# Performance work log

Hardware: AMD Instinct MI355X
Metric: run time of the kernel (lower is better)

## Reference

```python
import jax, jax.numpy as jnp
import numpy as np

N = 100000      # nodes
E = 1600000     # edges (avg degree 16)
D_IN, D_H, D_OUT = 128, 128, 64


def _pow(d, e):
    # torch code zeroes out inf from 0 ** negative_exponent
    p = jnp.power(d, e)
    return jnp.where(jnp.isinf(p), jnp.zeros_like(p), p)


def _gso_weights(params, deg, row, col):
    # params = [m1, m2, m3, e1, e2, e3, a]
    m1, m2, m3, e1, e2, e3, a = (params[i] for i in range(7))
    d = deg + a                       # self-loop-adjusted degrees, [N]
    pe2 = _pow(d, e2)
    pe3 = _pow(d, e3)
    w_edge = m2 * pe2[row] * pe3[col]                     # off-diagonal GSO entries, [E]
    w_self = m1 * _pow(d, e1) + m2 * pe2 * pe3 + m3       # diagonal GSO entries, [N]
    return w_edge, w_self


def setup_inputs() -> dict:
    key = jax.random.key(0)
    ks = jax.random.split(key, 8)
    x = jax.random.normal(ks[0], (N, D_IN), dtype=jnp.float32)
    edge_index = jax.random.randint(ks[1], (2, E), 0, N, dtype=jnp.int32)
    glorot = lambda k, i, o: jax.random.normal(k, (i, o), dtype=jnp.float32) * np.float32(np.sqrt(2.0 / (i + o)))
    W1 = glorot(ks[2], D_IN, D_H)
    W2 = glorot(ks[3], D_H, D_H)
    W3 = glorot(ks[4], D_H, D_OUT)
    b1 = jnp.zeros((D_H,), jnp.float32)
    b2 = jnp.zeros((D_H,), jnp.float32)
    b3 = jnp.zeros((D_OUT,), jnp.float32)
    # [m1, m2, m3, e1, e2, e3, a]
    gso1_params = jnp.array([0.0, 1.0, 0.0, 0.0, -0.5, -0.5, 1.0], jnp.float32)   # NORMADJ
    gso2_params = jnp.array([0.0, -1.0, 1.0, 0.0, -1.0, 0.0, 0.0], jnp.float32)   # RWLAPLACIAN
    return {"x": x, "edge_index": edge_index, "W1": W1, "b1": b1, "W2": W2,
            "b2": b2, "W3": W3, "b3": b3, "gso1_params": gso1_params,
            "gso2_params": gso2_params}


def reference(x, edge_index, W1, b1, W2, b2, W3, b3, gso1_params, gso2_params):
    row, col = edge_index[0], edge_index[1]
    deg = jax.ops.segment_sum(jnp.ones(row.shape, x.dtype), row, num_segments=N)
    we1, ws1 = _gso_weights(gso1_params, deg, row, col)
    we2, ws2 = _gso_weights(gso2_params, deg, row, col)
    w_edge = we1 + we2   # combined two-GSO edge weights, [E]
    w_self = ws1 + ws2   # combined diagonal (self-loop) weights, [N]

    def conv(h, W, b):
        h = h @ W                                                        # [N, d_out]
        agg = jax.ops.segment_sum(w_edge[:, None] * h[col], row, num_segments=N)
        return agg + w_self[:, None] * h + b

    h = jax.nn.relu(conv(x, W1, b1))
    h = jax.nn.relu(conv(h, W2, b2))   # dropout=0.0 (eval) -> identity
    return conv(h, W3, b3)
```

## Files before the change

kernel.cpp:

```cpp
#include <hip/hip_runtime.h>
#include <hip/hip_fp16.h>
#include <math.h>
#include <type_traits>

typedef _Float16 half8 __attribute__((ext_vector_type(8)));
typedef float floatx4 __attribute__((ext_vector_type(4)));

__global__ void deg_convert_kernel(const int* __restrict__ row, int* __restrict__ degi, int E,
                                   const float* __restrict__ W1, const float* __restrict__ W2,
                                   const float* __restrict__ W3, _Float16* __restrict__ Wt1,
                                   _Float16* __restrict__ Wt2, _Float16* __restrict__ Wt3,
                                   int degBlocks) {
    if ((int)blockIdx.x < degBlocks) {
        int g = blockIdx.x * 256 + threadIdx.x;
        if (g < E) atomicAdd(&degi[row[g]], 1);
    } else {
        int g = (blockIdx.x - degBlocks) * 256 + threadIdx.x;
        if (g < 16384) {
            int k = g >> 7, n = g & 127;
            Wt1[n * 128 + k] = (_Float16)W1[g];
        } else if (g < 32768) {
            int h = g - 16384; int k = h >> 7, n = h & 127;
            Wt2[n * 128 + k] = (_Float16)W2[h];
        } else if (g < 40960) {
            int h = g - 32768; int k = h >> 6, n = h & 63;
            Wt3[n * 128 + k] = (_Float16)W3[h];
        }
    }
}

__device__ __forceinline__ float pow_z(float d, float e) {
    float p = powf(d, e);
    return isinf(p) ? 0.0f : p;
}

__device__ __forceinline__ void gso_coeff(float deg, const float* __restrict__ p1,
                                          const float* __restrict__ p2,
                                          float4* cf, float* ws) {
    float m1a = p1[0], m2a = p1[1], m3a = p1[2], e1a = p1[3], e2a = p1[4], e3a = p1[5], aa = p1[6];
    float m1b = p2[0], m2b = p2[1], m3b = p2[2], e1b = p2[3], e2b = p2[4], e3b = p2[5], ab = p2[6];
    float d1 = deg + aa, d2 = deg + ab;
    float pa1 = pow_z(d1, e1a), pa2 = pow_z(d1, e2a), pa3 = pow_z(d1, e3a);
    float pb1 = pow_z(d2, e1b), pb2 = pow_z(d2, e2b), pb3 = pow_z(d2, e3b);
    *cf = make_float4(m2a * pa2, pa3, m2b * pb2, pb3);
    *ws = m1a * pa1 + m2a * pa2 * pa3 + m3a
        + m1b * pb1 + m2b * pb2 * pb3 + m3b;
}

__global__ void scan_block_kernel(const int* __restrict__ degi, int* __restrict__ rowptr,
                                  int* __restrict__ blocksum,
                                  const float* __restrict__ p1, const float* __restrict__ p2,
                                  float4* __restrict__ coeff, float* __restrict__ wself, int n) {
    __shared__ int sums[256];
    int tid = threadIdx.x;
    int base = blockIdx.x * 1024 + tid * 4;
    int d0 = (base + 0 < n) ? degi[base + 0] : 0;
    int d1 = (base + 1 < n) ? degi[base + 1] : 0;
    int d2 = (base + 2 < n) ? degi[base + 2] : 0;
    int d3 = (base + 3 < n) ? degi[base + 3] : 0;
    int s0 = d0, s1 = s0 + d1, s2 = s1 + d2, s3 = s2 + d3;
    sums[tid] = s3;
    __syncthreads();
    for (int off = 1; off < 256; off <<= 1) {
        int v = (tid >= off) ? sums[tid - off] : 0;
        __syncthreads();
        sums[tid] += v;
        __syncthreads();
    }
    int excl = sums[tid] - s3;
    if (base + 0 < n) rowptr[base + 1] = excl + s0;
    if (base + 1 < n) rowptr[base + 2] = excl + s1;
    if (base + 2 < n) rowptr[base + 3] = excl + s2;
    if (base + 3 < n) rowptr[base + 4] = excl + s3;
    if (tid == 255) blocksum[blockIdx.x] = sums[255];
    int dd[4] = {d0, d1, d2, d3};
#pragma unroll
    for (int u = 0; u < 4; ++u) {
        if (base + u < n) {
            float4 cf; float ws;
            gso_coeff((float)dd[u], p1, p2, &cf, &ws);
            coeff[base + u] = cf;
            wself[base + u] = ws;
        }
    }
}

__global__ void scan_add_kernel(int* __restrict__ rowptr, const int* __restrict__ blocksum,
                                int n, int nblk) {
    __shared__ int s[128];
    int tid = threadIdx.x;
    if (tid < 128) s[tid] = (tid < nblk) ? blocksum[tid] : 0;
    __syncthreads();
    for (int off = 1; off < 128; off <<= 1) {
        int v = 0;
        if (tid < 128 && tid >= off) v = s[tid - off];
        __syncthreads();
        if (tid < 128) s[tid] += v;
        __syncthreads();
    }
    int g = blockIdx.x * 256 + tid;
    if (g == 0) rowptr[0] = 0;
    if (g < n) {
        int b = g >> 10;
        int off = (b == 0) ? 0 : s[b - 1];
        rowptr[g + 1] += off;
    }
}

__global__ __launch_bounds__(256) void partition_kernel(
        const int* __restrict__ row, const int* __restrict__ col,
        const int* __restrict__ rowptr, int* __restrict__ gcur,
        const float4* __restrict__ coeff, int2* __restrict__ epack_mid,
        int E, int shift, int NB) {
    __shared__ int scnt[256], sofs[256], scur[256], gslot[256];
    __shared__ int2 sdata[4096];
    __shared__ unsigned short sbkt[4096];

    int tid = threadIdx.x;
    int base = blockIdx.x * 4096;
    scnt[tid] = 0;
    __syncthreads();

    int epk[16]; float ew[16]; int eb[16];
#pragma unroll
    for (int u = 0; u < 16; ++u) {
        int e = base + u * 256 + tid;
        eb[u] = -1;
        if (e < E) {
            int r = row[e], c = col[e];
            int b = r >> shift;
            eb[u] = b;
            atomicAdd(&scnt[b], 1);
            float4 cr = coeff[r], cc = coeff[c];
            ew[u] = cr.x * cc.y + cr.z * cc.w;
            epk[u] = c | ((r & ((1 << shift) - 1)) << 20);
        }
    }
    __syncthreads();
    sofs[tid] = scnt[tid];
    __syncthreads();
    for (int off = 1; off < 256; off <<= 1) {
        int v = (tid >= off) ? sofs[tid - off] : 0;
        __syncthreads();
        sofs[tid] += v;
        __syncthreads();
    }
    int excl = sofs[tid] - scnt[tid];
    sofs[tid] = excl;
    scur[tid] = excl;
    if (tid < NB && scnt[tid] > 0)
        gslot[tid] = rowptr[tid << shift] + atomicAdd(&gcur[tid], scnt[tid]);
    __syncthreads();
#pragma unroll
    for (int u = 0; u < 16; ++u) {
        if (eb[u] >= 0) {
            int idx = atomicAdd(&scur[eb[u]], 1);
            sdata[idx] = make_int2(epk[u], __float_as_int(ew[u]));
            sbkt[idx] = (unsigned short)eb[u];
        }
    }
    __syncthreads();
    int cntR = min(4096, E - base);
    for (int i = tid; i < cntR; i += 256) {
        int b = sbkt[i];
        epack_mid[gslot[b] + (i - sofs[b])] = sdata[i];
    }
}

__global__ __launch_bounds__(256) void bucket_sort_kernel(
        const int* __restrict__ rowptr, const int2* __restrict__ epack_mid,
        int2* __restrict__ epack, int N, int shift) {
    __shared__ int lcur[4096];
    int b = blockIdx.x;
    int tid = threadIdx.x;
    int rows = 1 << shift;
    int row0 = b << shift;
    for (int j = tid; j < rows; j += 256) {
        int rid = row0 + j;
        if (rid < N) lcur[j] = rowptr[rid];
    }
    __syncthreads();
    int slice0 = rowptr[row0];
    int slice1 = rowptr[min(row0 + rows, N)];
    for (int i = slice0 + tid; i < slice1; i += 256) {
        int2 p = epack_mid[i];
        int rl = ((unsigned)p.x) >> 20;
        int pos = atomicAdd(&lcur[rl], 1);
        epack[pos] = make_int2(p.x & 0xFFFFF, p.y);
    }
}

template<int TN, typename AT>
__global__ __launch_bounds__(256) void gemm_mfma(const AT* __restrict__ A,
        const _Float16* __restrict__ Wt, _Float16* __restrict__ C, int n) {
    constexpr int K = 128;
    constexpr int TM = 128;
    constexpr int LDK = K + 8;
    __shared__ _Float16 As[TM][LDK];
    __shared__ _Float16 Bs[TN][LDK];

    int tid = threadIdx.x;
    int wave = tid >> 6, lane = tid & 63;
    int q = lane >> 4, t = lane & 15;
    int rowbase = blockIdx.x * TM;

    if constexpr (std::is_same<AT, float>::value) {
        for (int i = tid; i < TM * K / 4; i += 256) {
            int r = i >> 5;
            int kc = (i & 31) * 4;
            int rr = rowbase + r;
            float4 v = make_float4(0.f, 0.f, 0.f, 0.f);
            if (rr < n) v = *(const float4*)&A[(size_t)rr * K + kc];
            As[r][kc + 0] = (_Float16)v.x;
            As[r][kc + 1] = (_Float16)v.y;
            As[r][kc + 2] = (_Float16)v.z;
            As[r][kc + 3] = (_Float16)v.w;
        }
    } else {
        for (int i = tid; i < TM * K / 8; i += 256) {
            int r = i >> 4;
            int kc = (i & 15) * 8;
            int rr = rowbase + r;
            uint4 v = make_uint4(0u, 0u, 0u, 0u);
            if (rr < n) v = *(const uint4*)&A[(size_t)rr * K + kc];
            *(uint4*)&As[r][kc] = v;
        }
    }
    for (int i = tid; i < TN * K / 8; i += 256) {
        int nr = i >> 4;
        int kc = (i & 15) * 8;
        *(uint4*)&Bs[nr][kc] = *(const uint4*)&Wt[(size_t)nr * K + kc];
    }
    __syncthreads();

    int m0 = wave * 32;
    floatx4 acc0[TN / 16], acc1[TN / 16];
#pragma unroll
    for (int nt = 0; nt < TN / 16; ++nt) {
        acc0[nt] = (floatx4){0.f, 0.f, 0.f, 0.f};
        acc1[nt] = (floatx4){0.f, 0.f, 0.f, 0.f};
    }

#pragma unroll
    for (int kk = 0; kk < K; kk += 32) {
        half8 a0 = *(const half8*)&As[m0 + t][kk + q * 8];
        half8 a1 = *(const half8*)&As[m0 + 16 + t][kk + q * 8];
#pragma unroll
        for (int nt = 0; nt < TN / 16; ++nt) {
            half8 b = *(const half8*)&Bs[nt * 16 + t][kk + q * 8];
            acc0[nt] = __builtin_amdgcn_mfma_f32_16x16x32_f16(a0, b, acc0[nt], 0, 0, 0);
            acc1[nt] = __builtin_amdgcn_mfma_f32_16x16x32_f16(a1, b, acc1[nt], 0, 0, 0);
        }
    }

#pragma unroll
    for (int nt = 0; nt < TN / 16; ++nt) {
#pragma unroll
        for (int r = 0; r < 4; ++r) {
            int rr0 = rowbase + m0 + q * 4 + r;
            if (rr0 < n) C[(size_t)rr0 * TN + nt * 16 + t] = (_Float16)acc0[nt][r];
            int rr1 = rr0 + 16;
            if (rr1 < n) C[(size_t)rr1 * TN + nt * 16 + t] = (_Float16)acc1[nt][r];
        }
    }
}

__global__ __launch_bounds__(256) void agg128_kernel(const __half2* __restrict__ H,
        const int* __restrict__ rowptr, const int2* __restrict__ epack,
        const float* __restrict__ wself, const float* __restrict__ bias,
        __half2* __restrict__ out, int n) {
    int node = blockIdx.x * 4 + (threadIdx.x >> 6);
    if (node >= n) return;
    int lane = threadIdx.x & 63;
    int start = rowptr[node], end = rowptr[node + 1];
    float ws = wself[node];
    float2 hs = __half22float2(H[(size_t)node * 64 + lane]);
    float ax = ws * hs.x, ay = ws * hs.y;
    int e = start;
    for (; e + 16 <= end; e += 16) {
        int2 p[16];
#pragma unroll
        for (int j = 0; j < 16; ++j) p[j] = epack[e + j];
        __half2 hh[16];
#pragma unroll
        for (int j = 0; j < 16; ++j) hh[j] = H[(size_t)p[j].x * 64 + lane];
#pragma unroll
        for (int j = 0; j < 16; ++j) {
            float w = __int_as_float(p[j].y);
            float2 f = __half22float2(hh[j]);
            ax += w * f.x; ay += w * f.y;
        }
    }
    if (e + 8 <= end) {
        int2 p[8];
#pragma unroll
        for (int j = 0; j < 8; ++j) p[j] = epack[e + j];
        __half2 hh[8];
#pragma unroll
        for (int j = 0; j < 8; ++j) hh[j] = H[(size_t)p[j].x * 64 + lane];
#pragma unroll
        for (int j = 0; j < 8; ++j) {
            float w = __int_as_float(p[j].y);
            float2 f = __half22float2(hh[j]);
            ax += w * f.x; ay += w * f.y;
        }
        e += 8;
    }
    if (e + 4 <= end) {
        int2 p[4];
#pragma unroll
        for (int j = 0; j < 4; ++j) p[j] = epack[e + j];
        __half2 hh[4];
#pragma unroll
        for (int j = 0; j < 4; ++j) hh[j] = H[(size_t)p[j].x * 64 + lane];
#pragma unroll
        for (int j = 0; j < 4; ++j) {
            float w = __int_as_float(p[j].y);
            float2 f = __half22float2(hh[j]);
            ax += w * f.x; ay += w * f.y;
        }
        e += 4;
    }
    for (; e < end; ++e) {
        int2 pe = epack[e];
        float w = __int_as_float(pe.y);
        float2 f = __half22float2(H[(size_t)pe.x * 64 + lane]);
        ax += w * f.x; ay += w * f.y;
    }
    float2 b = *(const float2*)&bias[2 * lane];
    float vx = fmaxf(ax + b.x, 0.0f);
    float vy = fmaxf(ay + b.y, 0.0f);
    out[(size_t)node * 64 + lane] = __floats2half2_rn(vx, vy);
}

__global__ __launch_bounds__(256) void agg64_kernel(const __half* __restrict__ H,
        const int* __restrict__ rowptr, const int2* __restrict__ epack,
        const float* __restrict__ wself, const float* __restrict__ bias,
        float* __restrict__ out, int n) {
    int node = blockIdx.x * 4 + (threadIdx.x >> 6);
    if (node >= n) return;
    int lane = threadIdx.x & 63;
    int start = rowptr[node], end = rowptr[node + 1];
    float ws = wself[node];
    float acc = ws * __half2float(H[(size_t)node * 64 + lane]);
    int e = start;
    for (; e + 16 <= end; e += 16) {
        int2 p[16];
#pragma unroll
        for (int j = 0; j < 16; ++j) p[j] = epack[e + j];
        float f[16];
#pragma unroll
        for (int j = 0; j < 16; ++j) f[j] = __half2float(H[(size_t)p[j].x * 64 + lane]);
#pragma unroll
        for (int j = 0; j < 16; ++j) acc += __int_as_float(p[j].y) * f[j];
    }
    if (e + 8 <= end) {
        int2 p[8];
#pragma unroll
        for (int j = 0; j < 8; ++j) p[j] = epack[e + j];
        float f[8];
#pragma unroll
        for (int j = 0; j < 8; ++j) f[j] = __half2float(H[(size_t)p[j].x * 64 + lane]);
#pragma unroll
        for (int j = 0; j < 8; ++j) acc += __int_as_float(p[j].y) * f[j];
        e += 8;
    }
    if (e + 4 <= end) {
        int2 p[4];
#pragma unroll
        for (int j = 0; j < 4; ++j) p[j] = epack[e + j];
        float f[4];
#pragma unroll
        for (int j = 0; j < 4; ++j) f[j] = __half2float(H[(size_t)p[j].x * 64 + lane]);
#pragma unroll
        for (int j = 0; j < 4; ++j) acc += __int_as_float(p[j].y) * f[j];
        e += 4;
    }
    for (; e < end; ++e) {
        int2 pe = epack[e];
        acc += __int_as_float(pe.y) * __half2float(H[(size_t)pe.x * 64 + lane]);
    }
    out[(size_t)node * 64 + lane] = acc + bias[lane];
}

extern "C" void kernel_launch(void* const* d_in, const int* in_sizes, int n_in,
                              void* d_out, int out_size, void* d_ws, size_t ws_size,
                              hipStream_t stream) {
    const float* x  = (const float*)d_in[0];
    const int*   ei = (const int*)d_in[1];
    const float* W1 = (const float*)d_in[2];
    const float* b1 = (const float*)d_in[3];
    const float* W2 = (const float*)d_in[4];
    const float* b2 = (const float*)d_in[5];
    const float* W3 = (const float*)d_in[6];
    const float* b3 = (const float*)d_in[7];
    const float* p1 = (const float*)d_in[8];
    const float* p2 = (const float*)d_in[9];

    const int N = in_sizes[0] / 128;
    const int E = in_sizes[1] / 2;
    const int* row = ei;
    const int* col = ei + E;

    int shift = 0;
    while ((((N - 1) >> shift) + 1) > 256) shift++;
    const int NB = ((N - 1) >> shift) + 1;

    char* p = (char*)d_ws;
    auto alloc = [&](size_t bytes) -> void* {
        void* q = (void*)p;
        p += (bytes + 255) & ~(size_t)255;
        return q;
    };
    int*      degi      = (int*)alloc((size_t)N * 4);
    int*      gcur      = (int*)alloc(256 * 4);
    int*      rowptr    = (int*)alloc((size_t)(N + 1) * 4);
    const int NBLK      = (N + 1023) / 1024;
    int*      blocksum  = (int*)alloc((size_t)NBLK * 4);
    float4*   coeff     = (float4*)alloc((size_t)N * 16);
    float*    wself     = (float*)alloc((size_t)N * 4);
    int2*     epack_mid = (int2*)alloc((size_t)E * 8);
    int2*     epack     = (int2*)alloc((size_t)E * 8);
    _Float16* Wt1       = (_Float16*)alloc(128 * 128 * 2);
    _Float16* Wt2       = (_Float16*)alloc(128 * 128 * 2);
    _Float16* Wt3       = (_Float16*)alloc(128 * 64 * 2);
    _Float16* bufH      = (_Float16*)alloc((size_t)N * 128 * 2);
    _Float16* actH      = (_Float16*)alloc((size_t)N * 128 * 2);
    (void)ws_size; (void)n_in;

    size_t zero_bytes = (size_t)((char*)rowptr - (char*)degi);
    hipMemsetAsync(degi, 0, zero_bytes, stream);

    const int degBlocks = (E + 255) / 256;
    deg_convert_kernel<<<degBlocks + 160, 256, 0, stream>>>(row, degi, E, W1, W2, W3,
                                                            Wt1, Wt2, Wt3, degBlocks);
    scan_block_kernel<<<NBLK, 256, 0, stream>>>(degi, rowptr, blocksum, p1, p2, coeff, wself, N);
    scan_add_kernel<<<(N + 255) / 256, 256, 0, stream>>>(rowptr, blocksum, N, NBLK);
    partition_kernel<<<(E + 4095) / 4096, 256, 0, stream>>>(row, col, rowptr, gcur, coeff,
                                                            epack_mid, E, shift, NB);
    bucket_sort_kernel<<<NB, 256, 0, stream>>>(rowptr, epack_mid, epack, N, shift);

    float* out = (float*)d_out;
    int aggGrid = (N + 3) / 4;
    int gemmGrid = (N + 127) / 128;
    gemm_mfma<128, float><<<gemmGrid, 256, 0, stream>>>(x, Wt1, bufH, N);
    agg128_kernel<<<aggGrid, 256, 0, stream>>>((const __half2*)bufH, rowptr, epack, wself,
                                               b1, (__half2*)actH, N);
    gemm_mfma<128, _Float16><<<gemmGrid, 256, 0, stream>>>(actH, Wt2, bufH, N);
    agg128_kernel<<<aggGrid, 256, 0, stream>>>((const __half2*)bufH, rowptr, epack, wself,
                                               b2, (__half2*)actH, N);
    gemm_mfma<64, _Float16><<<gemmGrid, 256, 0, stream>>>(actH, Wt3, bufH, N);
    agg64_kernel<<<aggGrid, 256, 0, stream>>>((const __half*)bufH, rowptr, epack, wself,
                                              b3, out, N);
}
```

Baseline: 487.2 us.

## Fuse first GEMM into setup kernel with degree count and weight conversion

After: 485.8 us. About the same (-0.3%).

```diff
diff --git a/kernel.cpp b/kernel.cpp
--- a/kernel.cpp
+++ b/kernel.cpp
@@ -6,27 +6,136 @@
 typedef _Float16 half8 __attribute__((ext_vector_type(8)));
 typedef float floatx4 __attribute__((ext_vector_type(4)));
 
-__global__ void deg_convert_kernel(const int* __restrict__ row, int* __restrict__ degi, int E,
-                                   const float* __restrict__ W1, const float* __restrict__ W2,
-                                   const float* __restrict__ W3, _Float16* __restrict__ Wt1,
-                                   _Float16* __restrict__ Wt2, _Float16* __restrict__ Wt3,
-                                   int degBlocks) {
-    if ((int)blockIdx.x < degBlocks) {
-        int g = blockIdx.x * 256 + threadIdx.x;
-        if (g < E) atomicAdd(&degi[row[g]], 1);
+template<int TN, typename AT, bool WFP32>
+__device__ __forceinline__ void gemm_body(const AT* __restrict__ A,
+        const void* __restrict__ Wsrc, _Float16* __restrict__ C, int n, int blk,
+        _Float16* lds) {
+    constexpr int K = 128;
+    constexpr int TM = 128;
+    constexpr int LDK = K + 8;
+    _Float16 (*As)[LDK] = (_Float16 (*)[LDK])lds;
+    _Float16 (*Bs)[LDK] = (_Float16 (*)[LDK])(lds + TM * LDK);
+
+    int tid = threadIdx.x;
+    int wave = tid >> 6, lane = tid & 63;
+    int q = lane >> 4, t = lane & 15;
+    int rowbase = blk * TM;
+
+    if constexpr (std::is_same<AT, float>::value) {
+        for (int i = tid; i < TM * K / 4; i += 256) {
+            int r = i >> 5;
+            int kc = (i & 31) * 4;
+            int rr = rowbase + r;
+            float4 v = make_float4(0.f, 0.f, 0.f, 0.f);
+            if (rr < n) v = *(const float4*)&A[(size_t)rr * K + kc];
+            As[r][kc + 0] = (_Float16)v.x;
+            As[r][kc + 1] = (_Float16)v.y;
+            As[r][kc + 2] = (_Float16)v.z;
+            As[r][kc + 3] = (_Float16)v.w;
+        }
     } else {
-        int g = (blockIdx.x - degBlocks) * 256 + threadIdx.x;
+        for (int i = tid; i < TM * K / 8; i += 256) {
+            int r = i >> 4;
+            int kc = (i & 15) * 8;
+            int rr = rowbase + r;
+            uint4 v = make_uint4(0u, 0u, 0u, 0u);
+            if (rr < n) v = *(const uint4*)&A[(size_t)rr * K + kc];
+            *(uint4*)&As[r][kc] = v;
+        }
+    }
+    if constexpr (WFP32) {
+        const float* W = (const float*)Wsrc;
+        for (int i = tid; i < K * TN / 4; i += 256) {
+            float4 v = *(const float4*)&W[i * 4];
+            int k = (i * 4) / TN, nn = (i * 4) % TN;
+            Bs[nn + 0][k] = (_Float16)v.x;
+            Bs[nn + 1][k] = (_Float16)v.y;
+            Bs[nn + 2][k] = (_Float16)v.z;
+            Bs[nn + 3][k] = (_Float16)v.w;
+        }
+    } else {
+        const _Float16* Wt = (const _Float16*)Wsrc;
+        for (int i = tid; i < TN * K / 8; i += 256) {
+            int nr = i >> 4;
+            int kc = (i & 15) * 8;
+            *(uint4*)&Bs[nr][kc] = *(const uint4*)&Wt[(size_t)nr * K + kc];
+        }
+    }
+    __syncthreads();
+
+    int m0 = wave * 32;
+    floatx4 acc0[TN / 16], acc1[TN / 16];
+#pragma unroll
+    for (int nt = 0; nt < TN / 16; ++nt) {
+        acc0[nt] = (floatx4){0.f, 0.f, 0.f, 0.f};
+        acc1[nt] = (floatx4){0.f, 0.f, 0.f, 0.f};
+    }
+
+#pragma unroll
+    for (int kk = 0; kk < K; kk += 32) {
+        half8 a0 = *(const half8*)&As[m0 + t][kk + q * 8];
+        half8 a1 = *(const half8*)&As[m0 + 16 + t][kk + q * 8];
+#pragma unroll
+        for (int nt = 0; nt < TN / 16; ++nt) {
+            half8 b = *(const half8*)&Bs[nt * 16 + t][kk + q * 8];
+            acc0[nt] = __builtin_amdgcn_mfma_f32_16x16x32_f16(a0, b, acc0[nt], 0, 0, 0);
+            acc1[nt] = __builtin_amdgcn_mfma_f32_16x16x32_f16(a1, b, acc1[nt], 0, 0, 0);
+        }
+    }
+
+#pragma unroll
+    for (int nt = 0; nt < TN / 16; ++nt) {
+#pragma unroll
+        for (int r = 0; r < 4; ++r) {
+            int rr0 = rowbase + m0 + q * 4 + r;
+            if (rr0 < n) C[(size_t)rr0 * TN + nt * 16 + t] = (_Float16)acc0[nt][r];
+            int rr1 = rr0 + 16;
+            if (rr1 < n) C[(size_t)rr1 * TN + nt * 16 + t] = (_Float16)acc1[nt][r];
+        }
+    }
+}
+
+__global__ __launch_bounds__(256) void setup_fused_kernel(
+        const float* __restrict__ x, const float* __restrict__ W1,
+        _Float16* __restrict__ bufH, int N,
+        const int* __restrict__ row, int* __restrict__ degi, int E,
+        const float* __restrict__ W2, const float* __restrict__ W3,
+        _Float16* __restrict__ Wt2, _Float16* __restrict__ Wt3,
+        int gemmBlocks, int degBlocks4) {
+    __shared__ _Float16 lds[(128 + 128) * 136];
+    int b = blockIdx.x;
+    if (b < gemmBlocks) {
+        gemm_body<128, float, true>(x, W1, bufH, N, b, lds);
+    } else if (b < gemmBlocks + degBlocks4) {
+        int e0 = (b - gemmBlocks) * 1024 + threadIdx.x * 4;
+        if (e0 + 3 < E) {
+            int4 r4 = *(const int4*)&row[e0];
+            atomicAdd(&degi[r4.x], 1);
+            atomicAdd(&degi[r4.y], 1);
+            atomicAdd(&degi[r4.z], 1);
+            atomicAdd(&degi[r4.w], 1);
+        } else {
+#pragma unroll
+            for (int j = 0; j < 4; ++j)
+                if (e0 + j < E) atomicAdd(&degi[row[e0 + j]], 1);
+        }
+    } else {
+        int g = (b - gemmBlocks - degBlocks4) * 256 + threadIdx.x;
         if (g < 16384) {
             int k = g >> 7, n = g & 127;
-            Wt1[n * 128 + k] = (_Float16)W1[g];
-        } else if (g < 32768) {
-            int h = g - 16384; int k = h >> 7, n = h & 127;
-            Wt2[n * 128 + k] = (_Float16)W2[h];
-        } else if (g < 40960) {
-            int h = g - 32768; int k = h >> 6, n = h & 63;
+            Wt2[n * 128 + k] = (_Float16)W2[g];
+        } else if (g < 24576) {
+            int h = g - 16384; int k = h >> 6, n = h & 63;
             Wt3[n * 128 + k] = (_Float16)W3[h];
         }
     }
+}
+
+template<int TN>
+__global__ __launch_bounds__(256) void gemm_mfma(const _Float16* __restrict__ A,
+        const _Float16* __restrict__ Wt, _Float16* __restrict__ C, int n) {
+    __shared__ _Float16 lds[(128 + TN) * 136];
+    gemm_body<TN, _Float16, false>(A, Wt, C, n, blockIdx.x, lds);
 }
 
 __device__ __forceinline__ float pow_z(float d, float e) {
@@ -112,7 +221,7 @@
         const int* __restrict__ rowptr, int* __restrict__ gcur,
         const float4* __restrict__ coeff, int2* __restrict__ epack_mid,
         int E, int shift, int NB) {
-    __shared__ int scnt[256], sofs[256], scur[256], gslot[256];
+    __shared__ int scnt[256], sofs[256], gslot[256];
     __shared__ int2 sdata[4096];
     __shared__ unsigned short sbkt[4096];
 
@@ -121,16 +230,30 @@
     scnt[tid] = 0;
     __syncthreads();
 
-    int epk[16]; float ew[16]; int eb[16];
-#pragma unroll
-    for (int u = 0; u < 16; ++u) {
-        int e = base + u * 256 + tid;
-        eb[u] = -1;
-        if (e < E) {
-            int r = row[e], c = col[e];
+    int epk[16]; float ew[16]; int eb[16]; int eidx[16];
+#pragma unroll
+    for (int v = 0; v < 4; ++v) {
+        int e0 = base + v * 1024 + tid * 4;
+        int4 r4, c4;
+        bool full = (e0 + 3 < E);
+        if (full) {
+            r4 = *(const int4*)&row[e0];
+            c4 = *(const int4*)&col[e0];
+        }
+#pragma unroll
+        for (int j = 0; j < 4; ++j) {
+            int u = v * 4 + j;
+            eb[u] = -1;
+            int r, c;
+            if (full) {
+                r = (&r4.x)[j]; c = (&c4.x)[j];
+            } else {
+                if (e0 + j >= E) continue;
+                r = row[e0 + j]; c = col[e0 + j];
+            }
             int b = r >> shift;
             eb[u] = b;
-            atomicAdd(&scnt[b], 1);
+            eidx[u] = atomicAdd(&scnt[b], 1);
             float4 cr = coeff[r], cc = coeff[c];
             ew[u] = cr.x * cc.y + cr.z * cc.w;
             epk[u] = c | ((r & ((1 << shift) - 1)) << 20);
@@ -147,14 +270,13 @@
     }
     int excl = sofs[tid] - scnt[tid];
     sofs[tid] = excl;
-    scur[tid] = excl;
     if (tid < NB && scnt[tid] > 0)
         gslot[tid] = rowptr[tid << shift] + atomicAdd(&gcur[tid], scnt[tid]);
     __syncthreads();
 #pragma unroll
     for (int u = 0; u < 16; ++u) {
         if (eb[u] >= 0) {
-            int idx = atomicAdd(&scur[eb[u]], 1);
+            int idx = sofs[eb[u]] + eidx[u];
             sdata[idx] = make_int2(epk[u], __float_as_int(ew[u]));
             sbkt[idx] = (unsigned short)eb[u];
         }
@@ -187,81 +309,6 @@
         int rl = ((unsigned)p.x) >> 20;
         int pos = atomicAdd(&lcur[rl], 1);
         epack[pos] = make_int2(p.x & 0xFFFFF, p.y);
-    }
-}
-
-template<int TN, typename AT>
-__global__ __launch_bounds__(256) void gemm_mfma(const AT* __restrict__ A,
-        const _Float16* __restrict__ Wt, _Float16* __restrict__ C, int n) {
-    constexpr int K = 128;
-    constexpr int TM = 128;
-    constexpr int LDK = K + 8;
-    __shared__ _Float16 As[TM][LDK];
-    __shared__ _Float16 Bs[TN][LDK];
-
-    int tid = threadIdx.x;
-    int wave = tid >> 6, lane = tid & 63;
-    int q = lane >> 4, t = lane & 15;
-    int rowbase = blockIdx.x * TM;
-
-    if constexpr (std::is_same<AT, float>::value) {
-        for (int i = tid; i < TM * K / 4; i += 256) {
-            int r = i >> 5;
-            int kc = (i & 31) * 4;
-            int rr = rowbase + r;
-            float4 v = make_float4(0.f, 0.f, 0.f, 0.f);
-            if (rr < n) v = *(const float4*)&A[(size_t)rr * K + kc];
-            As[r][kc + 0] = (_Float16)v.x;
-            As[r][kc + 1] = (_Float16)v.y;
-            As[r][kc + 2] = (_Float16)v.z;
-            As[r][kc + 3] = (_Float16)v.w;
-        }
-    } else {
-        for (int i = tid; i < TM * K / 8; i += 256) {
-            int r = i >> 4;
-            int kc = (i & 15) * 8;
-            int rr = rowbase + r;
-            uint4 v = make_uint4(0u, 0u, 0u, 0u);
-            if (rr < n) v = *(const uint4*)&A[(size_t)rr * K + kc];
-            *(uint4*)&As[r][kc] = v;
-        }
-    }
-    for (int i = tid; i < TN * K / 8; i += 256) {
-        int nr = i >> 4;
-        int kc = (i & 15) * 8;
-        *(uint4*)&Bs[nr][kc] = *(const uint4*)&Wt[(size_t)nr * K + kc];
-    }
-    __syncthreads();
-
-    int m0 = wave * 32;
-    floatx4 acc0[TN / 16], acc1[TN / 16];
-#pragma unroll
-    for (int nt = 0; nt < TN / 16; ++nt) {
-        acc0[nt] = (floatx4){0.f, 0.f, 0.f, 0.f};
-        acc1[nt] = (floatx4){0.f, 0.f, 0.f, 0.f};
-    }
-
-#pragma unroll
-    for (int kk = 0; kk < K; kk += 32) {
-        half8 a0 = *(const half8*)&As[m0 + t][kk + q * 8];
-        half8 a1 = *(const half8*)&As[m0 + 16 + t][kk + q * 8];
-#pragma unroll
-        for (int nt = 0; nt < TN / 16; ++nt) {
-            half8 b = *(const half8*)&Bs[nt * 16 + t][kk + q * 8];
-            acc0[nt] = __builtin_amdgcn_mfma_f32_16x16x32_f16(a0, b, acc0[nt], 0, 0, 0);
-            acc1[nt] = __builtin_amdgcn_mfma_f32_16x16x32_f16(a1, b, acc1[nt], 0, 0, 0);
-        }
-    }
-
-#pragma unroll
-    for (int nt = 0; nt < TN / 16; ++nt) {
-#pragma unroll
-        for (int r = 0; r < 4; ++r) {
-            int rr0 = rowbase + m0 + q * 4 + r;
-            if (rr0 < n) C[(size_t)rr0 * TN + nt * 16 + t] = (_Float16)acc0[nt][r];
-            int rr1 = rr0 + 16;
-            if (rr1 < n) C[(size_t)rr1 * TN + nt * 16 + t] = (_Float16)acc1[nt][r];
-        }
     }
 }
 
@@ -421,7 +468,6 @@
     float*    wself     = (float*)alloc((size_t)N * 4);
     int2*     epack_mid = (int2*)alloc((size_t)E * 8);
     int2*     epack     = (int2*)alloc((size_t)E * 8);
-    _Float16* Wt1       = (_Float16*)alloc(128 * 128 * 2);
     _Float16* Wt2       = (_Float16*)alloc(128 * 128 * 2);
     _Float16* Wt3       = (_Float16*)alloc(128 * 64 * 2);
     _Float16* bufH      = (_Float16*)alloc((size_t)N * 128 * 2);
@@ -431,9 +477,12 @@
     size_t zero_bytes = (size_t)((char*)rowptr - (char*)degi);
     hipMemsetAsync(degi, 0, zero_bytes, stream);
 
-    const int degBlocks = (E + 255) / 256;
-    deg_convert_kernel<<<degBlocks + 160, 256, 0, stream>>>(row, degi, E, W1, W2, W3,
-                                                            Wt1, Wt2, Wt3, degBlocks);
+    const int gemmGrid  = (N + 127) / 128;
+    const int degBlocks4 = (E + 1023) / 1024;
+    const int convBlocks = (24576 + 255) / 256;
+    setup_fused_kernel<<<gemmGrid + degBlocks4 + convBlocks, 256, 0, stream>>>(
+        x, W1, bufH, N, row, degi, E, W2, W3, Wt2, Wt3, gemmGrid, degBlocks4);
+
     scan_block_kernel<<<NBLK, 256, 0, stream>>>(degi, rowptr, blocksum, p1, p2, coeff, wself, N);
     scan_add_kernel<<<(N + 255) / 256, 256, 0, stream>>>(rowptr, blocksum, N, NBLK);
     partition_kernel<<<(E + 4095) / 4096, 256, 0, stream>>>(row, col, rowptr, gcur, coeff,
@@ -442,14 +491,12 @@
 
     float* out = (float*)d_out;
     int aggGrid = (N + 3) / 4;
-    int gemmGrid = (N + 127) / 128;
-    gemm_mfma<128, float><<<gemmGrid, 256, 0, stream>>>(x, Wt1, bufH, N);
     agg128_kernel<<<aggGrid, 256, 0, stream>>>((const __half2*)bufH, rowptr, epack, wself,
                                                b1, (__half2*)actH, N);
-    gemm_mfma<128, _Float16><<<gemmGrid, 256, 0, stream>>>(actH, Wt2, bufH, N);
+    gemm_mfma<128><<<gemmGrid, 256, 0, stream>>>(actH, Wt2, bufH, N);
     agg128_kernel<<<aggGrid, 256, 0, stream>>>((const __half2*)bufH, rowptr, epack, wself,
                                                b2, (__half2*)actH, N);
-    gemm_mfma<64, _Float16><<<gemmGrid, 256, 0, stream>>>(actH, Wt3, bufH, N);
+    gemm_mfma<64><<<gemmGrid, 256, 0, stream>>>(actH, Wt3, bufH, N);
     agg64_kernel<<<aggGrid, 256, 0, stream>>>((const __half*)bufH, rowptr, epack, wself,
                                               b3, out, N);
 }
```

## Restructure CSR build around coarse row-bucket histogram instead of per-node degree atomics

Applied to the files above, without the earlier changes.

Result: faster. 428.5 us (-12.0%).

```diff
diff --git a/kernel.cpp b/kernel.cpp
--- a/kernel.cpp
+++ b/kernel.cpp
@@ -6,27 +6,168 @@
 typedef _Float16 half8 __attribute__((ext_vector_type(8)));
 typedef float floatx4 __attribute__((ext_vector_type(4)));
 
-__global__ void deg_convert_kernel(const int* __restrict__ row, int* __restrict__ degi, int E,
-                                   const float* __restrict__ W1, const float* __restrict__ W2,
-                                   const float* __restrict__ W3, _Float16* __restrict__ Wt1,
-                                   _Float16* __restrict__ Wt2, _Float16* __restrict__ Wt3,
-                                   int degBlocks) {
-    if ((int)blockIdx.x < degBlocks) {
-        int g = blockIdx.x * 256 + threadIdx.x;
-        if (g < E) atomicAdd(&degi[row[g]], 1);
+#define RSHIFT 9
+
+__global__ __launch_bounds__(256) void hist_conv_kernel(
+        const int* __restrict__ row, int E, int* __restrict__ bucketsize,
+        const float* __restrict__ W1, const float* __restrict__ W2,
+        const float* __restrict__ W3, _Float16* __restrict__ Wt1,
+        _Float16* __restrict__ Wt2, _Float16* __restrict__ Wt3, int histBlocks) {
+    int tid = threadIdx.x;
+    if ((int)blockIdx.x < histBlocks) {
+        __shared__ int h[256];
+        h[tid] = 0;
+        __syncthreads();
+        int base = blockIdx.x * 16384;
+#pragma unroll
+        for (int it = 0; it < 16; ++it) {
+            int e0 = base + it * 1024 + tid * 4;
+            if (e0 + 3 < E) {
+                int4 r4 = *(const int4*)&row[e0];
+                atomicAdd(&h[r4.x >> RSHIFT], 1);
+                atomicAdd(&h[r4.y >> RSHIFT], 1);
+                atomicAdd(&h[r4.z >> RSHIFT], 1);
+                atomicAdd(&h[r4.w >> RSHIFT], 1);
+            } else {
+#pragma unroll
+                for (int j = 0; j < 4; ++j)
+                    if (e0 + j < E) atomicAdd(&h[row[e0 + j] >> RSHIFT], 1);
+            }
+        }
+        __syncthreads();
+        if (h[tid]) atomicAdd(&bucketsize[tid], h[tid]);
     } else {
-        int g = (blockIdx.x - degBlocks) * 256 + threadIdx.x;
+        int g = ((int)blockIdx.x - histBlocks) * 256 + tid;
         if (g < 16384) {
             int k = g >> 7, n = g & 127;
             Wt1[n * 128 + k] = (_Float16)W1[g];
         } else if (g < 32768) {
-            int h = g - 16384; int k = h >> 7, n = h & 127;
-            Wt2[n * 128 + k] = (_Float16)W2[h];
+            int h2 = g - 16384; int k = h2 >> 7, n = h2 & 127;
+            Wt2[n * 128 + k] = (_Float16)W2[h2];
         } else if (g < 40960) {
-            int h = g - 32768; int k = h >> 6, n = h & 63;
-            Wt3[n * 128 + k] = (_Float16)W3[h];
-        }
-    }
+            int h2 = g - 32768; int k = h2 >> 6, n = h2 & 63;
+            Wt3[n * 128 + k] = (_Float16)W3[h2];
+        }
+    }
+}
+
+__global__ void scan_buckets_kernel(const int* __restrict__ bucketsize,
+                                    int* __restrict__ bucketbase,
+                                    int* __restrict__ rowptr, int N, int E) {
+    __shared__ int s[256];
+    int tid = threadIdx.x;
+    int v = bucketsize[tid];
+    s[tid] = v;
+    __syncthreads();
+    for (int off = 1; off < 256; off <<= 1) {
+        int u = (tid >= off) ? s[tid - off] : 0;
+        __syncthreads();
+        s[tid] += u;
+        __syncthreads();
+    }
+    bucketbase[tid] = s[tid] - v;
+    if (tid == 255) bucketbase[256] = s[255];
+    if (tid == 0) rowptr[N] = E;
+}
+
+__global__ __launch_bounds__(256) void partition_kernel(
+        const int* __restrict__ row, const int* __restrict__ col,
+        const int* __restrict__ bucketbase, int* __restrict__ gcur,
+        int* __restrict__ emid, int E, int NB) {
+    __shared__ int scnt[256], sofs[256], gslot[256];
+    __shared__ int sdata[4096];
+    __shared__ unsigned short sbkt[4096];
+
+    int tid = threadIdx.x;
+    int base = blockIdx.x * 4096;
+    scnt[tid] = 0;
+    __syncthreads();
+
+    int epk[16]; int eb[16]; int eidx[16];
+#pragma unroll
+    for (int v = 0; v < 4; ++v) {
+        int e0 = base + v * 1024 + tid * 4;
+        int4 r4, c4;
+        bool full = (e0 + 3 < E);
+        if (full) {
+            r4 = *(const int4*)&row[e0];
+            c4 = *(const int4*)&col[e0];
+        }
+#pragma unroll
+        for (int j = 0; j < 4; ++j) {
+            int u = v * 4 + j;
+            eb[u] = -1;
+            int r, c;
+            if (full) {
+                r = (&r4.x)[j]; c = (&c4.x)[j];
+            } else {
+                if (e0 + j >= E) continue;
+                r = row[e0 + j]; c = col[e0 + j];
+            }
+            int b = r >> RSHIFT;
+            eb[u] = b;
+            eidx[u] = atomicAdd(&scnt[b], 1);
+            epk[u] = c | ((r & ((1 << RSHIFT) - 1)) << 20);
+        }
+    }
+    __syncthreads();
+    sofs[tid] = scnt[tid];
+    __syncthreads();
+    for (int off = 1; off < 256; off <<= 1) {
+        int v = (tid >= off) ? sofs[tid - off] : 0;
+        __syncthreads();
+        sofs[tid] += v;
+        __syncthreads();
+    }
+    int excl = sofs[tid] - scnt[tid];
+    sofs[tid] = excl;
+    if (tid < NB && scnt[tid] > 0)
+        gslot[tid] = bucketbase[tid] + atomicAdd(&gcur[tid], scnt[tid]);
+    __syncthreads();
+#pragma unroll
+    for (int u = 0; u < 16; ++u) {
+        if (eb[u] >= 0) {
+            int idx = sofs[eb[u]] + eidx[u];
+            sdata[idx] = epk[u];
+            sbkt[idx] = (unsigned short)eb[u];
+        }
+    }
+    __syncthreads();
+    int cntR = min(4096, E - base);
+    for (int i = tid; i < cntR; i += 256) {
+        int b = sbkt[i];
+        emid[gslot[b] + (i - sofs[b])] = sdata[i];
+    }
+}
+
+__global__ __launch_bounds__(256) void bucket_deg_kernel(
+        const int* __restrict__ bucketbase, const int* __restrict__ emid,
+        int* __restrict__ rowptr, int N) {
+    __shared__ int cnt[512];
+    __shared__ int ssum[256];
+    int b = blockIdx.x;
+    int tid = threadIdx.x;
+    int row0 = b << RSHIFT;
+    int nrows = min(512, N - row0);
+    cnt[tid] = 0; cnt[tid + 256] = 0;
+    __syncthreads();
+    int seg0 = bucketbase[b], seg1 = bucketbase[b + 1];
+    for (int i = seg0 + tid; i < seg1; i += 256)
+        atomicAdd(&cnt[((unsigned)emid[i]) >> 20], 1);
+    __syncthreads();
+    int a0 = cnt[2 * tid], a1 = cnt[2 * tid + 1];
+    int tsum = a0 + a1;
+    ssum[tid] = tsum;
+    __syncthreads();
+    for (int off = 1; off < 256; off <<= 1) {
+        int v = (tid >= off) ? ssum[tid - off] : 0;
+        __syncthreads();
+        ssum[tid] += v;
+        __syncthreads();
+    }
+    int excl = ssum[tid] - tsum;
+    if (2 * tid < nrows)     rowptr[row0 + 2 * tid]     = seg0 + excl;
+    if (2 * tid + 1 < nrows) rowptr[row0 + 2 * tid + 1] = seg0 + excl + a0;
 }
 
 __device__ __forceinline__ float pow_z(float d, float e) {
@@ -34,159 +175,51 @@
     return isinf(p) ? 0.0f : p;
 }
 
-__device__ __forceinline__ void gso_coeff(float deg, const float* __restrict__ p1,
-                                          const float* __restrict__ p2,
-                                          float4* cf, float* ws) {
+__global__ void node_coeff_kernel(const int* __restrict__ rowptr,
+                                  const float* __restrict__ p1, const float* __restrict__ p2,
+                                  float4* __restrict__ coeff, float* __restrict__ wself, int N) {
+    int g = blockIdx.x * blockDim.x + threadIdx.x;
+    if (g >= N) return;
+    float deg = (float)(rowptr[g + 1] - rowptr[g]);
     float m1a = p1[0], m2a = p1[1], m3a = p1[2], e1a = p1[3], e2a = p1[4], e3a = p1[5], aa = p1[6];
     float m1b = p2[0], m2b = p2[1], m3b = p2[2], e1b = p2[3], e2b = p2[4], e3b = p2[5], ab = p2[6];
     float d1 = deg + aa, d2 = deg + ab;
     float pa1 = pow_z(d1, e1a), pa2 = pow_z(d1, e2a), pa3 = pow_z(d1, e3a);
     float pb1 = pow_z(d2, e1b), pb2 = pow_z(d2, e2b), pb3 = pow_z(d2, e3b);
-    *cf = make_float4(m2a * pa2, pa3, m2b * pb2, pb3);
-    *ws = m1a * pa1 + m2a * pa2 * pa3 + m3a
-        + m1b * pb1 + m2b * pb2 * pb3 + m3b;
-}
-
-__global__ void scan_block_kernel(const int* __restrict__ degi, int* __restrict__ rowptr,
-                                  int* __restrict__ blocksum,
-                                  const float* __restrict__ p1, const float* __restrict__ p2,
-                                  float4* __restrict__ coeff, float* __restrict__ wself, int n) {
-    __shared__ int sums[256];
-    int tid = threadIdx.x;
-    int base = blockIdx.x * 1024 + tid * 4;
-    int d0 = (base + 0 < n) ? degi[base + 0] : 0;
-    int d1 = (base + 1 < n) ? degi[base + 1] : 0;
-    int d2 = (base + 2 < n) ? degi[base + 2] : 0;
-    int d3 = (base + 3 < n) ? degi[base + 3] : 0;
-    int s0 = d0, s1 = s0 + d1, s2 = s1 + d2, s3 = s2 + d3;
-    sums[tid] = s3;
-    __syncthreads();
-    for (int off = 1; off < 256; off <<= 1) {
-        int v = (tid >= off) ? sums[tid - off] : 0;
-        __syncthreads();
-        sums[tid] += v;
-        __syncthreads();
-    }
-    int excl = sums[tid] - s3;
-    if (base + 0 < n) rowptr[base + 1] = excl + s0;
-    if (base + 1 < n) rowptr[base + 2] = excl + s1;
-    if (base + 2 < n) rowptr[base + 3] = excl + s2;
-    if (base + 3 < n) rowptr[base + 4] = excl + s3;
-    if (tid == 255) blocksum[blockIdx.x] = sums[255];
-    int dd[4] = {d0, d1, d2, d3};
-#pragma unroll
-    for (int u = 0; u < 4; ++u) {
-        if (base + u < n) {
-            float4 cf; float ws;
-            gso_coeff((float)dd[u], p1, p2, &cf, &ws);
-            coeff[base + u] = cf;
-            wself[base + u] = ws;
-        }
-    }
-}
-
-__global__ void scan_add_kernel(int* __restrict__ rowptr, const int* __restrict__ blocksum,
-                                int n, int nblk) {
-    __shared__ int s[128];
-    int tid = threadIdx.x;
-    if (tid < 128) s[tid] = (tid < nblk) ? blocksum[tid] : 0;
-    __syncthreads();
-    for (int off = 1; off < 128; off <<= 1) {
-        int v = 0;
-        if (tid < 128 && tid >= off) v = s[tid - off];
-        __syncthreads();
-        if (tid < 128) s[tid] += v;
-        __syncthreads();
-    }
-    int g = blockIdx.x * 256 + tid;
-    if (g == 0) rowptr[0] = 0;
-    if (g < n) {
-        int b = g >> 10;
-        int off = (b == 0) ? 0 : s[b - 1];
-        rowptr[g + 1] += off;
-    }
-}
-
-__global__ __launch_bounds__(256) void partition_kernel(
-        const int* __restrict__ row, const int* __restrict__ col,
-        const int* __restrict__ rowptr, int* __restrict__ gcur,
-        const float4* __restrict__ coeff, int2* __restrict__ epack_mid,
-        int E, int shift, int NB) {
-    __shared__ int scnt[256], sofs[256], scur[256], gslot[256];
-    __shared__ int2 sdata[4096];
-    __shared__ unsigned short sbkt[4096];
-
-    int tid = threadIdx.x;
-    int base = blockIdx.x * 4096;
-    scnt[tid] = 0;
-    __syncthreads();
-
-    int epk[16]; float ew[16]; int eb[16];
-#pragma unroll
-    for (int u = 0; u < 16; ++u) {
-        int e = base + u * 256 + tid;
-        eb[u] = -1;
-        if (e < E) {
-            int r = row[e], c = col[e];
-            int b = r >> shift;
-            eb[u] = b;
-            atomicAdd(&scnt[b], 1);
-            float4 cr = coeff[r], cc = coeff[c];
-            ew[u] = cr.x * cc.y + cr.z * cc.w;
-            epk[u] = c | ((r & ((1 << shift) - 1)) << 20);
-        }
-    }
-    __syncthreads();
-    sofs[tid] = scnt[tid];
-    __syncthreads();
-    for (int off = 1; off < 256; off <<= 1) {
-        int v = (tid >= off) ? sofs[tid - off] : 0;
-        __syncthreads();
-        sofs[tid] += v;
-        __syncthreads();
-    }
-    int excl = sofs[tid] - scnt[tid];
-    sofs[tid] = excl;
-    scur[tid] = excl;
-    if (tid < NB && scnt[tid] > 0)
-        gslot[tid] = rowptr[tid << shift] + atomicAdd(&gcur[tid], scnt[tid]);
-    __syncthreads();
-#pragma unroll
-    for (int u = 0; u < 16; ++u) {
-        if (eb[u] >= 0) {
-            int idx = atomicAdd(&scur[eb[u]], 1);
-            sdata[idx] = make_int2(epk[u], __float_as_int(ew[u]));
-            sbkt[idx] = (unsigned short)eb[u];
-        }
-    }
-    __syncthreads();
-    int cntR = min(4096, E - base);
-    for (int i = tid; i < cntR; i += 256) {
-        int b = sbkt[i];
-        epack_mid[gslot[b] + (i - sofs[b])] = sdata[i];
-    }
-}
-
-__global__ __launch_bounds__(256) void bucket_sort_kernel(
-        const int* __restrict__ rowptr, const int2* __restrict__ epack_mid,
-        int2* __restrict__ epack, int N, int shift) {
-    __shared__ int lcur[4096];
+    coeff[g] = make_float4(m2a * pa2, pa3, m2b * pb2, pb3);
+    wself[g] = m1a * pa1 + m2a * pa2 * pa3 + m3a
+             + m1b * pb1 + m2b * pb2 * pb3 + m3b;
+}
+
+__global__ __launch_bounds__(256) void bucket_place_kernel(
+        const int* __restrict__ bucketbase, const int* __restrict__ emid,
+        const int* __restrict__ rowptr, const float4* __restrict__ coeff,
+        int2* __restrict__ epack, int N) {
+    __shared__ int lcur[512];
+    __shared__ float4 scoef[512];
     int b = blockIdx.x;
     int tid = threadIdx.x;
-    int rows = 1 << shift;
-    int row0 = b << shift;
-    for (int j = tid; j < rows; j += 256) {
-        int rid = row0 + j;
-        if (rid < N) lcur[j] = rowptr[rid];
-    }
-    __syncthreads();
-    int slice0 = rowptr[row0];
-    int slice1 = rowptr[min(row0 + rows, N)];
-    for (int i = slice0 + tid; i < slice1; i += 256) {
-        int2 p = epack_mid[i];
-        int rl = ((unsigned)p.x) >> 20;
+    int row0 = b << RSHIFT;
+    int nrows = min(512, N - row0);
+#pragma unroll
+    for (int u = 0; u < 2; ++u) {
+        int j = tid + u * 256;
+        if (j < nrows) {
+            lcur[j] = rowptr[row0 + j];
+            scoef[j] = coeff[row0 + j];
+        }
+    }
+    __syncthreads();
+    int seg0 = bucketbase[b], seg1 = bucketbase[b + 1];
+    for (int i = seg0 + tid; i < seg1; i += 256) {
+        int v = emid[i];
+        int rl = ((unsigned)v) >> 20;
+        int c = v & 0xFFFFF;
+        float4 cr = scoef[rl];
+        float4 cc = coeff[c];
+        float w = cr.x * cc.y + cr.z * cc.w;
         int pos = atomicAdd(&lcur[rl], 1);
-        epack[pos] = make_int2(p.x & 0xFFFFF, p.y);
+        epack[pos] = make_int2(c, __float_as_int(w));
     }
 }
 
@@ -401,10 +434,7 @@
     const int E = in_sizes[1] / 2;
     const int* row = ei;
     const int* col = ei + E;
-
-    int shift = 0;
-    while ((((N - 1) >> shift) + 1) > 256) shift++;
-    const int NB = ((N - 1) >> shift) + 1;
+    const int NB = ((N - 1) >> RSHIFT) + 1;
 
     char* p = (char*)d_ws;
     auto alloc = [&](size_t bytes) -> void* {
@@ -412,33 +442,33 @@
         p += (bytes + 255) & ~(size_t)255;
         return q;
     };
-    int*      degi      = (int*)alloc((size_t)N * 4);
-    int*      gcur      = (int*)alloc(256 * 4);
-    int*      rowptr    = (int*)alloc((size_t)(N + 1) * 4);
-    const int NBLK      = (N + 1023) / 1024;
-    int*      blocksum  = (int*)alloc((size_t)NBLK * 4);
-    float4*   coeff     = (float4*)alloc((size_t)N * 16);
-    float*    wself     = (float*)alloc((size_t)N * 4);
-    int2*     epack_mid = (int2*)alloc((size_t)E * 8);
-    int2*     epack     = (int2*)alloc((size_t)E * 8);
-    _Float16* Wt1       = (_Float16*)alloc(128 * 128 * 2);
-    _Float16* Wt2       = (_Float16*)alloc(128 * 128 * 2);
-    _Float16* Wt3       = (_Float16*)alloc(128 * 64 * 2);
-    _Float16* bufH      = (_Float16*)alloc((size_t)N * 128 * 2);
-    _Float16* actH      = (_Float16*)alloc((size_t)N * 128 * 2);
+    int*      bucketsize = (int*)alloc(256 * 4);
+    int*      gcur       = (int*)alloc(256 * 4);
+    int*      bucketbase = (int*)alloc(257 * 4);
+    int*      rowptr     = (int*)alloc((size_t)(N + 1) * 4);
+    float4*   coeff      = (float4*)alloc((size_t)N * 16);
+    float*    wself      = (float*)alloc((size_t)N * 4);
+    int*      emid       = (int*)alloc((size_t)E * 4);
+    int2*     epack      = (int2*)alloc((size_t)E * 8);
+    _Float16* Wt1        = (_Float16*)alloc(128 * 128 * 2);
+    _Float16* Wt2        = (_Float16*)alloc(128 * 128 * 2);
+    _Float16* Wt3        = (_Float16*)alloc(128 * 64 * 2);
+    _Float16* bufH       = (_Float16*)alloc((size_t)N * 128 * 2);
+    _Float16* actH       = (_Float16*)alloc((size_t)N * 128 * 2);
     (void)ws_size; (void)n_in;
 
-    size_t zero_bytes = (size_t)((char*)rowptr - (char*)degi);
-    hipMemsetAsync(degi, 0, zero_bytes, stream);
-
-    const int degBlocks = (E + 255) / 256;
-    deg_convert_kernel<<<degBlocks + 160, 256, 0, stream>>>(row, degi, E, W1, W2, W3,
-                                                            Wt1, Wt2, Wt3, degBlocks);
-    scan_block_kernel<<<NBLK, 256, 0, stream>>>(degi, rowptr, blocksum, p1, p2, coeff, wself, N);
-    scan_add_kernel<<<(N + 255) / 256, 256, 0, stream>>>(rowptr, blocksum, N, NBLK);
-    partition_kernel<<<(E + 4095) / 4096, 256, 0, stream>>>(row, col, rowptr, gcur, coeff,
-                                                            epack_mid, E, shift, NB);
-    bucket_sort_kernel<<<NB, 256, 0, stream>>>(rowptr, epack_mid, epack, N, shift);
+    hipMemsetAsync(bucketsize, 0, 512 * 4, stream);
+
+    const int histBlocks = (E + 16383) / 16384;
+    const int convBlocks = (40960 + 255) / 256;
+    hist_conv_kernel<<<histBlocks + convBlocks, 256, 0, stream>>>(
+        row, E, bucketsize, W1, W2, W3, Wt1, Wt2, Wt3, histBlocks);
+    scan_buckets_kernel<<<1, 256, 0, stream>>>(bucketsize, bucketbase, rowptr, N, E);
+    partition_kernel<<<(E + 4095) / 4096, 256, 0, stream>>>(row, col, bucketbase, gcur,
+                                                            emid, E, NB);
+    bucket_deg_kernel<<<NB, 256, 0, stream>>>(bucketbase, emid, rowptr, N);
+    node_coeff_kernel<<<(N + 255) / 256, 256, 0, stream>>>(rowptr, p1, p2, coeff, wself, N);
+    bucket_place_kernel<<<NB, 256, 0, stream>>>(bucketbase, emid, rowptr, coeff, epack, N);
 
     float* out = (float*)d_out;
     int aggGrid = (N + 3) / 4;
```
